# Optimization experiments

Hardware: AMD Instinct MI355X
Metric: run time of the kernel (lower is better)

The kernel has to match this reference:

```python
import jax, jax.numpy as jnp
import numpy as np
from jax import lax

EPS = 1e-4
THRESHOLD = 0.0


@jax.custom_vjp
def ternary(x):
    return jnp.where(x <= -THRESHOLD, -1.0,
                     jnp.where(x >= THRESHOLD, 1.0, 0.0)).astype(x.dtype)


def _ternary_fwd(x):
    return ternary(x), x


def _ternary_bwd(x, g):
    # STE: pass gradient where -1 < x < 1, zero where |x| >= 1
    mask = (x < 1.0) & (x > -1.0)
    return (g * mask.astype(g.dtype),)


ternary.defvjp(_ternary_fwd, _ternary_bwd)


def setup_inputs() -> dict:
    key = jax.random.key(0)
    k1, k2, k3 = jax.random.split(key, 3)
    N, C_in, H, W = 32, 256, 56, 56
    C_out, K = 256, 3
    x = jax.random.normal(k1, (N, C_in, H, W), dtype=jnp.float32)
    gamma = jnp.ones((C_in,), dtype=jnp.float32)
    beta = jnp.zeros((C_in,), dtype=jnp.float32)
    fan_in = C_in * K * K
    weight = jax.random.normal(k2, (C_out, C_in, K, K), dtype=jnp.float32) / np.sqrt(fan_in)
    bias = jax.random.normal(k3, (C_out,), dtype=jnp.float32) * 0.01
    return {"x": x, "gamma": gamma, "beta": beta, "weight": weight, "bias": bias}


def reference(x, gamma, beta, weight, bias):
    # BatchNorm2d (training mode: batch statistics, biased var), eps=1e-4
    mean = jnp.mean(x, axis=(0, 2, 3), keepdims=True)
    var = jnp.mean(jnp.square(x - mean), axis=(0, 2, 3), keepdims=True)
    xn = (x - mean) * lax.rsqrt(var + EPS)
    xn = xn * gamma[None, :, None, None] + beta[None, :, None, None]
    # Ternarize to {-1, 0, 1}
    t = ternary(xn)
    # Conv2d stride=1, padding=1 (NCHW / OIHW)
    y = lax.conv_general_dilated(
        t, weight, window_strides=(1, 1), padding=[(1, 1), (1, 1)],
        dimension_numbers=("NCHW", "OIHW", "NCHW"))
    y = y + bias[None, :, None, None]
    return jax.nn.relu(y)
```

## Files before the change

### kernel.cpp

```cpp
#include <hip/hip_runtime.h>
#include <stdint.h>

#define NN 32
#define CI 256
#define CO 256
#define HH 56
#define WW 56
#define TPH 58
#define TPW 72
#define CNT (NN*HH*WW)

typedef int i32x4 __attribute__((ext_vector_type(4)));

__device__ __forceinline__ void gld16(const void* g, void* l) {
    __builtin_amdgcn_global_load_lds(
        (const __attribute__((address_space(1))) void*)(uintptr_t)g,
        (__attribute__((address_space(3))) void*)(uint32_t)(uintptr_t)l,
        16, 0, 0);
}

__global__ void stats_part(const float* __restrict__ x, double* __restrict__ part) {
    const int c = blockIdx.x, sp = blockIdx.y;
    double s = 0.0, ss = 0.0;
    const size_t base = ((size_t)(sp * 4) * CI + c) * 3136;
    for (int idx = threadIdx.x; idx < 4 * 784; idx += 256) {
        int nl = idx / 784, q = idx % 784;
        const float4 v = *(const float4*)(x + base + (size_t)nl * CI * 3136 + q * 4);
        double a = v.x, b = v.y, cc = v.z, d = v.w;
        s  += (a + b) + (cc + d);
        ss += (a * a + b * b) + (cc * cc + d * d);
    }
    for (int off = 32; off > 0; off >>= 1) {
        s  += __shfl_down(s, off, 64);
        ss += __shfl_down(ss, off, 64);
    }
    __shared__ double red[8];
    int wid = threadIdx.x >> 6, lane = threadIdx.x & 63;
    if (lane == 0) { red[wid] = s; red[4 + wid] = ss; }
    __syncthreads();
    if (threadIdx.x == 0) {
        part[(sp * 256 + c) * 2]     = (red[0] + red[1]) + (red[2] + red[3]);
        part[(sp * 256 + c) * 2 + 1] = (red[4] + red[5]) + (red[6] + red[7]);
    }
}

__global__ void stats_final(const double* __restrict__ part,
                            const float* __restrict__ gamma,
                            const float* __restrict__ beta,
                            double* __restrict__ stats) {
    const int c = threadIdx.x;
    double S = 0.0, SS = 0.0;
    for (int sp = 0; sp < 8; ++sp) {
        S  += part[(sp * 256 + c) * 2];
        SS += part[(sp * 256 + c) * 2 + 1];
    }
    double mean = S / (double)CNT;
    double var  = SS / (double)CNT - mean * mean;
    double invstd = 1.0 / sqrt(var + 1e-4);
    double scale = (double)gamma[c] * invstd;
    double shift = (double)beta[c] - mean * scale;
    stats[2 * c]     = scale;
    stats[2 * c + 1] = shift;
}

__global__ void wtrans_kernel(const float* __restrict__ w,
                              int8_t* __restrict__ wT,
                              float* __restrict__ qscale) {
    const int co = blockIdx.x;
    const float* wp = w + (size_t)co * 2304;
    float v[9], m = 0.f;
#pragma unroll
    for (int it = 0; it < 9; ++it) {
        v[it] = wp[threadIdx.x + it * 256];
        m = fmaxf(m, fabsf(v[it]));
    }
    for (int off = 32; off > 0; off >>= 1) m = fmaxf(m, __shfl_down(m, off, 64));
    __shared__ float red[4];
    __shared__ float qsh;
    int wid = threadIdx.x >> 6, lane = threadIdx.x & 63;
    if (lane == 0) red[wid] = m;
    __syncthreads();
    if (threadIdx.x == 0) {
        float mx = fmaxf(fmaxf(red[0], red[1]), fmaxf(red[2], red[3]));
        float q = (mx > 0.f) ? mx / 127.f : 1.f;
        qsh = q;
        qscale[co] = q;
    }
    __syncthreads();
    const float q = qsh;
#pragma unroll
    for (int it = 0; it < 9; ++it) {
        int idx = threadIdx.x + it * 256;
        int ci = idx / 9, tap = idx % 9;
        int chunk = ci >> 6, cis = ci & 63;
        int iq = __float2int_rn(v[it] / q);
        iq = iq > 127 ? 127 : (iq < -127 ? -127 : iq);
        wT[((size_t)(tap * 4 + chunk) * 256 + co) * 64 + cis] = (int8_t)iq;
    }
}

__global__ void halo_kernel(int8_t* __restrict__ tp) {
    const int b = blockIdx.x, n = b >> 1, r = (b & 1) * 57;
    i32x4* dst = (i32x4*)(tp + ((size_t)n * TPH + r) * TPW * CI);
    const i32x4 z = {0, 0, 0, 0};
    for (int p = threadIdx.x; p < TPW * CI / 16; p += 256) dst[p] = z;
}

__global__ void ternarize_kernel(const float* __restrict__ x,
                                 const double* __restrict__ stats,
                                 int8_t* __restrict__ tp) {
    const int h = blockIdx.x, n = blockIdx.y;
    __shared__ int8_t L[56 * 260];
    const size_t xb = ((size_t)n * CI) * 3136 + (size_t)h * 56;
    for (int idx = threadIdx.x; idx < CI * 56; idx += 256) {
        int ci = idx / 56, w = idx - ci * 56;
        float val = x[xb + (size_t)ci * 3136 + w];
        double sc = stats[2 * ci], sh = stats[2 * ci + 1];
        L[w * 260 + ci] = (fma(sc, (double)val, sh) > 0.0) ? (int8_t)1 : (int8_t)-1;
    }
    __syncthreads();
    i32x4* rowp = (i32x4*)(tp + ((size_t)n * TPH + h + 1) * TPW * CI);
    for (int p = threadIdx.x; p < TPW * 16; p += 256) {
        int wo = p >> 4, c16 = p & 15;
        i32x4 v = {0, 0, 0, 0};
        if (wo >= 1 && wo <= 56) {
            const int* lp = (const int*)&L[(wo - 1) * 260 + c16 * 16];
            v.x = lp[0]; v.y = lp[1]; v.z = lp[2]; v.w = lp[3];
        }
        rowp[p] = v;
    }
}

__device__ __forceinline__ void stage_chunk(const int8_t* __restrict__ g0,
                                            int8_t* lbuf, int chunk, int tid) {
#pragma unroll
    for (int j = 0; j < 5; ++j) {
        int p = tid + j * 256;
        if (j < 4 || tid < 128) {
            int row = p / 288, rem = p - row * 288;
            int wp = rem >> 2, s = rem & 3;
            int g = (s - wp) & 3;
            gld16(g0 + (size_t)row * TPW * CI + wp * 256 + chunk * 64 + g * 16,
                  lbuf + p * 16);
        }
    }
}

__launch_bounds__(256, 2)
__global__ void conv_kernel(const int8_t* __restrict__ wT,
                            const int8_t* __restrict__ tp,
                            const float* __restrict__ bias,
                            const float* __restrict__ qscale,
                            float* __restrict__ out) {
    const int co_t = blockIdx.x;
    const int h0   = blockIdx.y * 2;
    const int n    = blockIdx.z;
    const int tid  = threadIdx.x;
    const int lane = tid & 63, wid = tid >> 6;
    const int l15 = lane & 15, qd = lane >> 4;
    const int m_off = (wid & 1) * 64;
    const int rowsel = wid >> 1;

    __shared__ int8_t Bsh[2 * 4 * TPW * 64];

    i32x4 acc[4][4];
#pragma unroll
    for (int i = 0; i < 4; ++i)
#pragma unroll
        for (int j = 0; j < 4; ++j) acc[i][j] = (i32x4){0, 0, 0, 0};

    const int8_t* g0 = tp + ((size_t)n * TPH + h0) * TPW * CI;

    stage_chunk(g0, Bsh, 0, tid);
    for (int c = 0; c < 4; ++c) {
        __syncthreads();
        if (c < 3) stage_chunk(g0, Bsh + ((c + 1) & 1) * 18432, c + 1, tid);
        const int8_t* lb = Bsh + (c & 1) * 18432;
#pragma unroll
        for (int kh = 0; kh < 3; ++kh) {
            const int brow = (rowsel + kh) * TPW;
#pragma unroll
            for (int kw = 0; kw < 3; ++kw) {
                const int tap = kh * 3 + kw;
                const i32x4* ap = (const i32x4*)(wT +
                    ((size_t)(tap * 4 + c) * 256 + co_t * 128 + m_off) * 64);
                i32x4 a[4], b[4];
#pragma unroll
                for (int i = 0; i < 4; ++i)
                    a[i] = ap[(i * 16 + l15) * 4 + qd];
#pragma unroll
                for (int j = 0; j < 4; ++j) {
                    int wp = j * 16 + l15 + kw;
                    int slot = (qd + wp) & 3;
                    b[j] = *(const i32x4*)&lb[(brow + wp) * 64 + slot * 16];
                }
#pragma unroll
                for (int i = 0; i < 4; ++i)
#pragma unroll
                    for (int j = 0; j < 4; ++j)
                        acc[i][j] = __builtin_amdgcn_mfma_i32_16x16x64_i8(
                            a[i], b[j], acc[i][j], 0, 0, 0);
            }
        }
    }

    const int h_out = h0 + rowsel;
#pragma unroll
    for (int i = 0; i < 4; ++i) {
        const int co = co_t * 128 + m_off + i * 16 + qd * 4;
        const float4 bv = *(const float4*)&bias[co];
        const float4 qv = *(const float4*)&qscale[co];
        const float bb[4] = {bv.x, bv.y, bv.z, bv.w};
        const float qq[4] = {qv.x, qv.y, qv.z, qv.w};
#pragma unroll
        for (int j = 0; j < 4; ++j) {
            const int w = j * 16 + l15;
            if (w < 56) {
                const size_t ob = (((size_t)n * CO + co) * HH + h_out) * WW + w;
#pragma unroll
                for (int r = 0; r < 4; ++r) {
                    float v = (float)acc[i][j][r] * qq[r] + bb[r];
                    out[ob + (size_t)r * (HH * WW)] = v > 0.f ? v : 0.f;
                }
            }
        }
    }
}

extern "C" void kernel_launch(void* const* d_in, const int* in_sizes, int n_in,
                              void* d_out, int out_size, void* d_ws, size_t ws_size,
                              hipStream_t stream) {
    const float* x      = (const float*)d_in[0];
    const float* gamma  = (const float*)d_in[1];
    const float* beta   = (const float*)d_in[2];
    const float* weight = (const float*)d_in[3];
    const float* bias   = (const float*)d_in[4];
    float* out = (float*)d_out;

    double* part    = (double*)d_ws;
    double* stats   = (double*)((char*)d_ws + 32768);
    float*  qscale  = (float*) ((char*)d_ws + 36864);
    int8_t* wT      = (int8_t*)((char*)d_ws + 65536);
    int8_t* tp      = (int8_t*)((char*)d_ws + 1048576);

    wtrans_kernel<<<256, 256, 0, stream>>>(weight, wT, qscale);
    halo_kernel<<<64, 256, 0, stream>>>(tp);
    stats_part<<<dim3(256, 8), 256, 0, stream>>>(x, part);
    stats_final<<<1, 256, 0, stream>>>(part, gamma, beta, stats);
    ternarize_kernel<<<dim3(HH, NN), 256, 0, stream>>>(x, stats, tp);
    conv_kernel<<<dim3(2, 28, NN), 256, 0, stream>>>(wT, tp, bias, qscale, out);
}
```

Before: 326.2 us.

## Tile four output rows per conv block and fold stats/halo into ternarize

The conv kernel now computes four output rows per block instead of two. Each wave holds two rows of accumulators, so every weight fragment loaded feeds twice as many MFMAs and the staged input halo shrinks relative to the useful rows. MFMA sections are bracketed with setprio. Separately, the stats_final and halo kernels are folded into the ternarize kernel, which now also loads x as float4. This removes two launches, at the cost of every block recomputing the per-channel stats and higher register and LDS pressure in conv.

```diff
diff --git a/kernel.cpp b/kernel.cpp
--- a/kernel.cpp
+++ b/kernel.cpp
@@ -44,25 +44,6 @@
     }
 }
 
-__global__ void stats_final(const double* __restrict__ part,
-                            const float* __restrict__ gamma,
-                            const float* __restrict__ beta,
-                            double* __restrict__ stats) {
-    const int c = threadIdx.x;
-    double S = 0.0, SS = 0.0;
-    for (int sp = 0; sp < 8; ++sp) {
-        S  += part[(sp * 256 + c) * 2];
-        SS += part[(sp * 256 + c) * 2 + 1];
-    }
-    double mean = S / (double)CNT;
-    double var  = SS / (double)CNT - mean * mean;
-    double invstd = 1.0 / sqrt(var + 1e-4);
-    double scale = (double)gamma[c] * invstd;
-    double shift = (double)beta[c] - mean * scale;
-    stats[2 * c]     = scale;
-    stats[2 * c + 1] = shift;
-}
-
 __global__ void wtrans_kernel(const float* __restrict__ w,
                               int8_t* __restrict__ wT,
                               float* __restrict__ qscale) {
@@ -99,27 +80,49 @@
     }
 }
 
-__global__ void halo_kernel(int8_t* __restrict__ tp) {
-    const int b = blockIdx.x, n = b >> 1, r = (b & 1) * 57;
-    i32x4* dst = (i32x4*)(tp + ((size_t)n * TPH + r) * TPW * CI);
-    const i32x4 z = {0, 0, 0, 0};
-    for (int p = threadIdx.x; p < TPW * CI / 16; p += 256) dst[p] = z;
-}
-
 __global__ void ternarize_kernel(const float* __restrict__ x,
-                                 const double* __restrict__ stats,
+                                 const double* __restrict__ part,
+                                 const float* __restrict__ gamma,
+                                 const float* __restrict__ beta,
                                  int8_t* __restrict__ tp) {
     const int h = blockIdx.x, n = blockIdx.y;
+    i32x4* rowp = (i32x4*)(tp + ((size_t)n * TPH + h) * TPW * CI);
+    if (h == 0 || h == TPH - 1) {
+        const i32x4 z = {0, 0, 0, 0};
+        for (int p = threadIdx.x; p < TPW * 16; p += 256) rowp[p] = z;
+        return;
+    }
+    __shared__ double Ssc[256], Ssh[256];
+    {
+        const int c = threadIdx.x;
+        double S = 0.0, SS = 0.0;
+#pragma unroll
+        for (int sp = 0; sp < 8; ++sp) {
+            S  += part[(sp * 256 + c) * 2];
+            SS += part[(sp * 256 + c) * 2 + 1];
+        }
+        double mean = S / (double)CNT;
+        double var  = SS / (double)CNT - mean * mean;
+        double invstd = 1.0 / sqrt(var + 1e-4);
+        double scale = (double)gamma[c] * invstd;
+        Ssc[c] = scale;
+        Ssh[c] = (double)beta[c] - mean * scale;
+    }
     __shared__ int8_t L[56 * 260];
-    const size_t xb = ((size_t)n * CI) * 3136 + (size_t)h * 56;
-    for (int idx = threadIdx.x; idx < CI * 56; idx += 256) {
-        int ci = idx / 56, w = idx - ci * 56;
-        float val = x[xb + (size_t)ci * 3136 + w];
-        double sc = stats[2 * ci], sh = stats[2 * ci + 1];
-        L[w * 260 + ci] = (fma(sc, (double)val, sh) > 0.0) ? (int8_t)1 : (int8_t)-1;
-    }
-    __syncthreads();
-    i32x4* rowp = (i32x4*)(tp + ((size_t)n * TPH + h + 1) * TPW * CI);
+    __syncthreads();
+    const int hin = h - 1;
+    const size_t xb = ((size_t)n * CI) * 3136 + (size_t)hin * 56;
+    for (int idx = threadIdx.x; idx < CI * 14; idx += 256) {
+        int ci = idx / 14, w4 = idx - ci * 14;
+        const float4 v = *(const float4*)(x + xb + (size_t)ci * 3136 + w4 * 4);
+        const double sc = Ssc[ci], sh = Ssh[ci];
+        const int w = w4 * 4;
+        L[(w + 0) * 260 + ci] = (fma(sc, (double)v.x, sh) > 0.0) ? (int8_t)1 : (int8_t)-1;
+        L[(w + 1) * 260 + ci] = (fma(sc, (double)v.y, sh) > 0.0) ? (int8_t)1 : (int8_t)-1;
+        L[(w + 2) * 260 + ci] = (fma(sc, (double)v.z, sh) > 0.0) ? (int8_t)1 : (int8_t)-1;
+        L[(w + 3) * 260 + ci] = (fma(sc, (double)v.w, sh) > 0.0) ? (int8_t)1 : (int8_t)-1;
+    }
+    __syncthreads();
     for (int p = threadIdx.x; p < TPW * 16; p += 256) {
         int wo = p >> 4, c16 = p & 15;
         i32x4 v = {0, 0, 0, 0};
@@ -131,12 +134,14 @@
     }
 }
 
-__device__ __forceinline__ void stage_chunk(const int8_t* __restrict__ g0,
-                                            int8_t* lbuf, int chunk, int tid) {
-#pragma unroll
-    for (int j = 0; j < 5; ++j) {
+#define CONV_LDS (6 * TPW * 64)
+
+__device__ __forceinline__ void stage6(const int8_t* __restrict__ g0,
+                                       int8_t* lbuf, int chunk, int tid) {
+#pragma unroll
+    for (int j = 0; j < 7; ++j) {
         int p = tid + j * 256;
-        if (j < 4 || tid < 128) {
+        if (j < 6 || tid < 192) {
             int row = p / 288, rem = p - row * 288;
             int wp = rem >> 2, s = rem & 3;
             int g = (s - wp) & 3;
@@ -153,58 +158,65 @@
                             const float* __restrict__ qscale,
                             float* __restrict__ out) {
     const int co_t = blockIdx.x;
-    const int h0   = blockIdx.y * 2;
+    const int h0   = blockIdx.y * 4;
     const int n    = blockIdx.z;
     const int tid  = threadIdx.x;
     const int lane = tid & 63, wid = tid >> 6;
     const int l15 = lane & 15, qd = lane >> 4;
     const int m_off = (wid & 1) * 64;
-    const int rowsel = wid >> 1;
-
-    __shared__ int8_t Bsh[2 * 4 * TPW * 64];
-
-    i32x4 acc[4][4];
+    const int rs = (wid >> 1) * 2;
+
+    __shared__ __align__(16) int8_t Bsh[2 * CONV_LDS];
+
+    i32x4 acc[4][4][2];
 #pragma unroll
     for (int i = 0; i < 4; ++i)
 #pragma unroll
-        for (int j = 0; j < 4; ++j) acc[i][j] = (i32x4){0, 0, 0, 0};
+        for (int j = 0; j < 4; ++j)
+#pragma unroll
+            for (int r = 0; r < 2; ++r) acc[i][j][r] = (i32x4){0, 0, 0, 0};
 
     const int8_t* g0 = tp + ((size_t)n * TPH + h0) * TPW * CI;
 
-    stage_chunk(g0, Bsh, 0, tid);
+    stage6(g0, Bsh, 0, tid);
     for (int c = 0; c < 4; ++c) {
         __syncthreads();
-        if (c < 3) stage_chunk(g0, Bsh + ((c + 1) & 1) * 18432, c + 1, tid);
-        const int8_t* lb = Bsh + (c & 1) * 18432;
+        if (c < 3) stage6(g0, Bsh + ((c + 1) & 1) * CONV_LDS, c + 1, tid);
+        const int8_t* lb = Bsh + (c & 1) * CONV_LDS;
 #pragma unroll
         for (int kh = 0; kh < 3; ++kh) {
-            const int brow = (rowsel + kh) * TPW;
 #pragma unroll
             for (int kw = 0; kw < 3; ++kw) {
                 const int tap = kh * 3 + kw;
                 const i32x4* ap = (const i32x4*)(wT +
                     ((size_t)(tap * 4 + c) * 256 + co_t * 128 + m_off) * 64);
-                i32x4 a[4], b[4];
+                i32x4 a[4], b[4][2];
 #pragma unroll
                 for (int i = 0; i < 4; ++i)
                     a[i] = ap[(i * 16 + l15) * 4 + qd];
 #pragma unroll
                 for (int j = 0; j < 4; ++j) {
-                    int wp = j * 16 + l15 + kw;
-                    int slot = (qd + wp) & 3;
-                    b[j] = *(const i32x4*)&lb[(brow + wp) * 64 + slot * 16];
+                    const int wp = j * 16 + l15 + kw;
+                    const int slot = (qd + wp) & 3;
+#pragma unroll
+                    for (int r = 0; r < 2; ++r)
+                        b[j][r] = *(const i32x4*)&lb[((rs + r + kh) * TPW + wp) * 64 + slot * 16];
                 }
+                __builtin_amdgcn_s_setprio(1);
 #pragma unroll
                 for (int i = 0; i < 4; ++i)
 #pragma unroll
                     for (int j = 0; j < 4; ++j)
-                        acc[i][j] = __builtin_amdgcn_mfma_i32_16x16x64_i8(
-                            a[i], b[j], acc[i][j], 0, 0, 0);
+#pragma unroll
+                        for (int r = 0; r < 2; ++r)
+                            acc[i][j][r] = __builtin_amdgcn_mfma_i32_16x16x64_i8(
+                                a[i], b[j][r], acc[i][j][r], 0, 0, 0);
+                __builtin_amdgcn_s_setprio(0);
             }
         }
     }
 
-    const int h_out = h0 + rowsel;
+    const int h_out = h0 + rs;
 #pragma unroll
     for (int i = 0; i < 4; ++i) {
         const int co = co_t * 128 + m_off + i * 16 + qd * 4;
@@ -216,11 +228,14 @@
         for (int j = 0; j < 4; ++j) {
             const int w = j * 16 + l15;
             if (w < 56) {
-                const size_t ob = (((size_t)n * CO + co) * HH + h_out) * WW + w;
-#pragma unroll
-                for (int r = 0; r < 4; ++r) {
-                    float v = (float)acc[i][j][r] * qq[r] + bb[r];
-                    out[ob + (size_t)r * (HH * WW)] = v > 0.f ? v : 0.f;
+#pragma unroll
+                for (int rr = 0; rr < 2; ++rr) {
+                    const size_t ob = (((size_t)n * CO + co) * HH + (h_out + rr)) * WW + w;
+#pragma unroll
+                    for (int r = 0; r < 4; ++r) {
+                        float v = (float)acc[i][j][rr][r] * qq[r] + bb[r];
+                        out[ob + (size_t)r * (HH * WW)] = v > 0.f ? v : 0.f;
+                    }
                 }
             }
         }
@@ -238,15 +253,12 @@
     float* out = (float*)d_out;
 
     double* part    = (double*)d_ws;
-    double* stats   = (double*)((char*)d_ws + 32768);
     float*  qscale  = (float*) ((char*)d_ws + 36864);
     int8_t* wT      = (int8_t*)((char*)d_ws + 65536);
     int8_t* tp      = (int8_t*)((char*)d_ws + 1048576);
 
     wtrans_kernel<<<256, 256, 0, stream>>>(weight, wT, qscale);
-    halo_kernel<<<64, 256, 0, stream>>>(tp);
     stats_part<<<dim3(256, 8), 256, 0, stream>>>(x, part);
-    stats_final<<<1, 256, 0, stream>>>(part, gamma, beta, stats);
-    ternarize_kernel<<<dim3(HH, NN), 256, 0, stream>>>(x, stats, tp);
-    conv_kernel<<<dim3(2, 28, NN), 256, 0, stream>>>(wT, tp, bias, qscale, out);
-}
+    ternarize_kernel<<<dim3(TPH, NN), 256, 0, stream>>>(x, part, gamma, beta, tp);
+    conv_kernel<<<dim3(2, 14, NN), 256, 0, stream>>>(wT, tp, bias, qscale, out);
+}
```

Measured after the change: 316.1 us. 3.1% less time.

## Fuse BN finalize and halo zeroing into ternarize; chunk-major padded layout

Applied to the files above, without the earlier changes.

Removes the stats_final and halo_kernel launches. Each ternarize block now recomputes per-channel scale and shift from the partial sums into shared memory, and the border rows are handled by extra blocks in the ternarize grid. Loads of x are vectorised to float4. The padded activation buffer moves to a chunk-major layout (64-channel chunks contiguous per row), and the conv staging addresses are updated to match, giving more contiguous global loads. The cost is redundant stats finalisation in every block.

```diff
diff --git a/kernel.cpp b/kernel.cpp
--- a/kernel.cpp
+++ b/kernel.cpp
@@ -44,25 +44,6 @@
     }
 }
 
-__global__ void stats_final(const double* __restrict__ part,
-                            const float* __restrict__ gamma,
-                            const float* __restrict__ beta,
-                            double* __restrict__ stats) {
-    const int c = threadIdx.x;
-    double S = 0.0, SS = 0.0;
-    for (int sp = 0; sp < 8; ++sp) {
-        S  += part[(sp * 256 + c) * 2];
-        SS += part[(sp * 256 + c) * 2 + 1];
-    }
-    double mean = S / (double)CNT;
-    double var  = SS / (double)CNT - mean * mean;
-    double invstd = 1.0 / sqrt(var + 1e-4);
-    double scale = (double)gamma[c] * invstd;
-    double shift = (double)beta[c] - mean * scale;
-    stats[2 * c]     = scale;
-    stats[2 * c + 1] = shift;
-}
-
 __global__ void wtrans_kernel(const float* __restrict__ w,
                               int8_t* __restrict__ wT,
                               float* __restrict__ qscale) {
@@ -99,27 +80,49 @@
     }
 }
 
-__global__ void halo_kernel(int8_t* __restrict__ tp) {
-    const int b = blockIdx.x, n = b >> 1, r = (b & 1) * 57;
-    i32x4* dst = (i32x4*)(tp + ((size_t)n * TPH + r) * TPW * CI);
-    const i32x4 z = {0, 0, 0, 0};
-    for (int p = threadIdx.x; p < TPW * CI / 16; p += 256) dst[p] = z;
-}
-
 __global__ void ternarize_kernel(const float* __restrict__ x,
-                                 const double* __restrict__ stats,
+                                 const double* __restrict__ part,
+                                 const float* __restrict__ gamma,
+                                 const float* __restrict__ beta,
                                  int8_t* __restrict__ tp) {
     const int h = blockIdx.x, n = blockIdx.y;
+    i32x4* rowp = (i32x4*)(tp + ((size_t)n * TPH + h) * TPW * CI);
+    if (h == 0 || h == TPH - 1) {
+        const i32x4 z = {0, 0, 0, 0};
+        for (int p = threadIdx.x; p < TPW * 16; p += 256) rowp[p] = z;
+        return;
+    }
+    __shared__ double Ssc[256], Ssh[256];
+    {
+        const int c = threadIdx.x;
+        double S = 0.0, SS = 0.0;
+#pragma unroll
+        for (int sp = 0; sp < 8; ++sp) {
+            S  += part[(sp * 256 + c) * 2];
+            SS += part[(sp * 256 + c) * 2 + 1];
+        }
+        double mean = S / (double)CNT;
+        double var  = SS / (double)CNT - mean * mean;
+        double invstd = 1.0 / sqrt(var + 1e-4);
+        double scale = (double)gamma[c] * invstd;
+        Ssc[c] = scale;
+        Ssh[c] = (double)beta[c] - mean * scale;
+    }
     __shared__ int8_t L[56 * 260];
-    const size_t xb = ((size_t)n * CI) * 3136 + (size_t)h * 56;
-    for (int idx = threadIdx.x; idx < CI * 56; idx += 256) {
-        int ci = idx / 56, w = idx - ci * 56;
-        float val = x[xb + (size_t)ci * 3136 + w];
-        double sc = stats[2 * ci], sh = stats[2 * ci + 1];
-        L[w * 260 + ci] = (fma(sc, (double)val, sh) > 0.0) ? (int8_t)1 : (int8_t)-1;
-    }
-    __syncthreads();
-    i32x4* rowp = (i32x4*)(tp + ((size_t)n * TPH + h + 1) * TPW * CI);
+    __syncthreads();
+    const int hin = h - 1;
+    const size_t xb = ((size_t)n * CI) * 3136 + (size_t)hin * 56;
+    for (int idx = threadIdx.x; idx < CI * 14; idx += 256) {
+        int ci = idx / 14, w4 = idx - ci * 14;
+        const float4 v = *(const float4*)(x + xb + (size_t)ci * 3136 + w4 * 4);
+        const double sc = Ssc[ci], sh = Ssh[ci];
+        const int w = w4 * 4;
+        L[(w + 0) * 260 + ci] = (fma(sc, (double)v.x, sh) > 0.0) ? (int8_t)1 : (int8_t)-1;
+        L[(w + 1) * 260 + ci] = (fma(sc, (double)v.y, sh) > 0.0) ? (int8_t)1 : (int8_t)-1;
+        L[(w + 2) * 260 + ci] = (fma(sc, (double)v.z, sh) > 0.0) ? (int8_t)1 : (int8_t)-1;
+        L[(w + 3) * 260 + ci] = (fma(sc, (double)v.w, sh) > 0.0) ? (int8_t)1 : (int8_t)-1;
+    }
+    __syncthreads();
     for (int p = threadIdx.x; p < TPW * 16; p += 256) {
         int wo = p >> 4, c16 = p & 15;
         i32x4 v = {0, 0, 0, 0};
@@ -127,7 +130,8 @@
             const int* lp = (const int*)&L[(wo - 1) * 260 + c16 * 16];
             v.x = lp[0]; v.y = lp[1]; v.z = lp[2]; v.w = lp[3];
         }
-        rowp[p] = v;
+        const int chunk = c16 >> 2, s = c16 & 3;
+        rowp[chunk * 288 + wo * 4 + s] = v;
     }
 }
 
@@ -140,7 +144,7 @@
             int row = p / 288, rem = p - row * 288;
             int wp = rem >> 2, s = rem & 3;
             int g = (s - wp) & 3;
-            gld16(g0 + (size_t)row * TPW * CI + wp * 256 + chunk * 64 + g * 16,
+            gld16(g0 + (size_t)row * TPW * CI + chunk * (TPW * 64) + wp * 64 + g * 16,
                   lbuf + p * 16);
         }
     }
@@ -238,15 +242,12 @@
     float* out = (float*)d_out;
 
     double* part    = (double*)d_ws;
-    double* stats   = (double*)((char*)d_ws + 32768);
     float*  qscale  = (float*) ((char*)d_ws + 36864);
     int8_t* wT      = (int8_t*)((char*)d_ws + 65536);
     int8_t* tp      = (int8_t*)((char*)d_ws + 1048576);
 
     wtrans_kernel<<<256, 256, 0, stream>>>(weight, wT, qscale);
-    halo_kernel<<<64, 256, 0, stream>>>(tp);
     stats_part<<<dim3(256, 8), 256, 0, stream>>>(x, part);
-    stats_final<<<1, 256, 0, stream>>>(part, gamma, beta, stats);
-    ternarize_kernel<<<dim3(HH, NN), 256, 0, stream>>>(x, stats, tp);
+    ternarize_kernel<<<dim3(TPH, NN), 256, 0, stream>>>(x, part, gamma, beta, tp);
     conv_kernel<<<dim3(2, 28, NN), 256, 0, stream>>>(wT, tp, bias, qscale, out);
 }
```

Result: no change. 322.9 us (-1.0%).
